# Optimization experiments

Measured on AMD Instinct MI355X. Metric: run time of the kernel, lower is better.

Reference implementation:

```python
import jax, jax.numpy as jnp
import numpy as np

N_NODES = 50000
N_EDGES = 600000
D_IN = 128
D_OUT = 128
P_DROP = 0.1
BN_EPS = 1e-5


def setup_inputs() -> dict:
    key = jax.random.key(0)
    ks = jax.random.split(key, 6)
    x = jax.random.normal(ks[0], (N_NODES, D_IN), dtype=jnp.float32)
    weight = jax.random.normal(ks[1], (D_IN, D_OUT), dtype=jnp.float32) * (1.0 / np.sqrt(D_IN))
    bias = jnp.zeros((D_OUT,), dtype=jnp.float32)
    gamma = jnp.ones((D_OUT,), dtype=jnp.float32)
    beta = jnp.zeros((D_OUT,), dtype=jnp.float32)
    dropout_u = jax.random.uniform(ks[2], (N_NODES, D_OUT), dtype=jnp.float32)
    edge_index = jax.random.randint(ks[3], (2, N_EDGES), 0, N_NODES, dtype=jnp.int64)
    return {"x": x, "weight": weight, "bias": bias, "gamma": gamma,
            "beta": beta, "dropout_u": dropout_u, "edge_index": edge_index}


def reference(x, weight, bias, gamma, beta, dropout_u, edge_index):
    N = x.shape[0]
    # --- GCNConv (add_self_loops=True, symmetric normalization) ---
    loop = jnp.arange(N, dtype=edge_index.dtype)
    src = jnp.concatenate([edge_index[0], loop])  # [E+N]
    dst = jnp.concatenate([edge_index[1], loop])  # [E+N]
    xw = x @ weight                               # [N, D_OUT] small GEMM
    deg = jnp.zeros((N,), dtype=xw.dtype).at[dst].add(1.0)
    dinv = jnp.where(deg > 0, jax.lax.rsqrt(jnp.maximum(deg, 1.0)), 0.0)
    norm = dinv[src] * dinv[dst]                  # [E+N]
    msgs = xw[src] * norm[:, None]                # gather: [E+N, D_OUT]
    z = jax.ops.segment_sum(msgs, dst, num_segments=N) + bias
    # --- activation -> BatchNorm (training stats) -> dropout ---
    z = jax.nn.relu(z)
    mean = jnp.mean(z, axis=0)
    var = jnp.mean((z - mean) ** 2, axis=0)       # biased var, as BN uses
    z = (z - mean) * jax.lax.rsqrt(var + BN_EPS) * gamma + beta
    keep = (dropout_u > P_DROP).astype(z.dtype)
    z = z * keep * (1.0 / (1.0 - P_DROP))
    return z.astype(x.dtype)
```

## Files before the change

kernel.cpp:

```cpp
#include <hip/hip_runtime.h>
#include <cstdint>
#include <cstddef>

#define D 128
#define P_DROP 0.1f
#define INV_KEEP (1.0f / 0.9f)
#define BN_EPS 1e-5f

typedef __attribute__((ext_vector_type(8))) short bf16x8;
typedef __attribute__((ext_vector_type(4))) float f32x4;

__device__ __forceinline__ unsigned f2bf(float f) {
    unsigned u = __float_as_uint(f);
    return (u + 0x7fffu + ((u >> 16) & 1u)) >> 16;
}
__device__ __forceinline__ float bf_lo(unsigned v) { return __uint_as_float(v << 16); }
__device__ __forceinline__ float bf_hi(unsigned v) { return __uint_as_float(v & 0xffff0000u); }

__global__ void k_init(int* __restrict__ hist, int N,
                       float* __restrict__ bnacc,
                       unsigned short* __restrict__ xwb) {
    int stride = gridDim.x * blockDim.x;
    int i0 = blockIdx.x * blockDim.x + threadIdx.x;
    for (int i = i0; i < N; i += stride) hist[i] = 0;
    for (int i = i0; i < 2048; i += stride) bnacc[i] = 0.f;
    if (i0 < 64) ((unsigned*)(xwb + (size_t)N * D))[i0] = 0u;
}

__global__ void k_hist(const int* __restrict__ dst, int* __restrict__ hist, int E) {
    int i = blockIdx.x * blockDim.x + threadIdx.x;
    if (i < E) atomicAdd(&hist[dst[i]], 1);
}

__global__ void k_scanA(const int* __restrict__ hist, int* __restrict__ tmp,
                        int* __restrict__ blocksum, int N) {
    __shared__ int sd[256];
    int tid = threadIdx.x;
    int i = blockIdx.x * 256 + tid;
    sd[tid] = (i < N) ? ((hist[i] + 7) & ~7) : 0;
    __syncthreads();
    for (int o = 1; o < 256; o <<= 1) {
        int t = (tid >= o) ? sd[tid - o] : 0;
        __syncthreads();
        sd[tid] += t;
        __syncthreads();
    }
    tmp[i] = sd[tid];
    if (tid == 255) blocksum[blockIdx.x] = sd[255];
}

__global__ void k_scanBC(const int* __restrict__ tmp, const int* __restrict__ blocksum,
                         const int* __restrict__ hist,
                         int* __restrict__ rowptr, int* __restrict__ cursor,
                         unsigned short* __restrict__ ssrc,
                         int N, int NBLK, int sent) {
    __shared__ int sd[256];
    int tid = threadIdx.x;
    int b = blockIdx.x;
    sd[tid] = (tid < NBLK && tid < b) ? blocksum[tid] : 0;
    __syncthreads();
    for (int o = 128; o > 0; o >>= 1) {
        if (tid < o) sd[tid] += sd[tid + o];
        __syncthreads();
    }
    int boff = sd[0];
    int i = b * 256 + tid;
    if (i < N) {
        int deg = hist[i];
        int pd = (deg + 7) & ~7;
        int r = tmp[i] + boff - pd;
        rowptr[i] = r;
        cursor[i] = r;
        for (int k = deg; k < pd; ++k) ssrc[r + k] = (unsigned short)sent;
    }
}

__global__ void k_place(const int* __restrict__ src, const int* __restrict__ dst,
                        int* __restrict__ cursor, unsigned short* __restrict__ ssrc, int E) {
    int i = blockIdx.x * blockDim.x + threadIdx.x;
    if (i < E) {
        int d = dst[i];
        int p = atomicAdd(&cursor[d], 1);
        ssrc[p] = (unsigned short)src[i];
    }
}

__global__ __launch_bounds__(256) void k_gemm(
    const float* __restrict__ x, const float* __restrict__ w,
    const int* __restrict__ hist, unsigned short* __restrict__ xwb,
    float* __restrict__ dinv, int N) {
    __shared__ unsigned short xs[64][136];
    __shared__ unsigned short wt[128][136];
    int tid = threadIdx.x;
    int row0 = blockIdx.x * 64;

#pragma unroll
    for (int i = 0; i < 32; ++i) {
        int flat = tid + i * 256;
        int n = flat & 127;
        int kp = flat >> 7;
        float a0 = w[(size_t)(2 * kp) * D + n];
        float a1 = w[(size_t)(2 * kp + 1) * D + n];
        *(unsigned*)&wt[n][2 * kp] = f2bf(a0) | (f2bf(a1) << 16);
    }
#pragma unroll
    for (int i = 0; i < 8; ++i) {
        int flat = tid + i * 256;
        int r = flat >> 5;
        int kq = flat & 31;
        int row = row0 + r;
        float4 v = (row < N) ? *(const float4*)&x[(size_t)row * D + kq * 4]
                             : make_float4(0.f, 0.f, 0.f, 0.f);
        uint2 pk;
        pk.x = f2bf(v.x) | (f2bf(v.y) << 16);
        pk.y = f2bf(v.z) | (f2bf(v.w) << 16);
        *(uint2*)&xs[r][kq * 4] = pk;
    }
    __syncthreads();

    int wv = tid >> 6, lane = tid & 63;
    int l15 = lane & 15, quad = lane >> 4;
    int mrow = wv * 16 + l15;
    f32x4 acc[8];
#pragma unroll
    for (int t = 0; t < 8; ++t) acc[t] = (f32x4){0.f, 0.f, 0.f, 0.f};
#pragma unroll
    for (int k0 = 0; k0 < D; k0 += 32) {
        bf16x8 af = *(bf16x8*)&xs[mrow][k0 + quad * 8];
#pragma unroll
        for (int nt = 0; nt < 8; ++nt) {
            bf16x8 bfr = *(bf16x8*)&wt[nt * 16 + l15][k0 + quad * 8];
            acc[nt] = __builtin_amdgcn_mfma_f32_16x16x32_bf16(af, bfr, acc[nt], 0, 0, 0);
        }
    }
#pragma unroll
    for (int reg = 0; reg < 4; ++reg) {
        int node = row0 + wv * 16 + quad * 4 + reg;
        if (node < N) {
            float dv = rsqrtf((float)(hist[node] + 1));
            if (l15 == 0) dinv[node] = dv;
#pragma unroll
            for (int nt = 0; nt < 8; ++nt) {
                float val = acc[nt][reg] * dv;
                xwb[(size_t)node * D + nt * 16 + l15] = (unsigned short)f2bf(val);
            }
        }
    }
}

__global__ __launch_bounds__(256) void k_aggregate(
    const unsigned short* __restrict__ xwb, const float* __restrict__ dinv,
    const unsigned short* __restrict__ ssrc, const int* __restrict__ rowptr,
    const int* __restrict__ hist, const float* __restrict__ bias,
    float* __restrict__ y, float* __restrict__ bnacc, int N) {
    int tid = threadIdx.x;
    int lane = tid & 63;
    int wv = tid >> 6;
    int w0 = blockIdx.x * 4 + wv;
    int totw = gridDim.x * 4;
    float2 b2 = *(const float2*)(bias + lane * 2);
    float s0 = 0.f, s1 = 0.f, q0 = 0.f, q1 = 0.f;

    int n = w0;
    int baseC = 0, degC = 0, vsC = 0;
    if (n < N) {
        baseC = rowptr[n];
        degC = hist[n];
        vsC = (int)ssrc[baseC + lane];
    }
    int np = n + totw;
    int baseP = 0, degP = 0;
    if (np < N) { baseP = rowptr[np]; degP = hist[np]; }

    while (n < N) {
        int nn = __builtin_amdgcn_readfirstlane(n);
        int vsP = 0;
        if (np < N) vsP = (int)ssrc[baseP + lane];
        int n2 = np + totw;
        int base2 = 0, deg2 = 0;
        if (n2 < N) { base2 = rowptr[n2]; deg2 = hist[n2]; }
        unsigned sv = *(const unsigned*)(xwb + (size_t)nn * D + lane * 2);
        int pdeg = (degC + 7) & ~7;
        float a0 = 0.f, a1 = 0.f;
        int lim0 = min(64, pdeg);
        for (int j0 = 0; j0 < lim0; j0 += 8) {
            unsigned vr[8];
#pragma unroll
            for (int j = 0; j < 8; ++j) {
                int idx = __builtin_amdgcn_readlane(vsC, j0 + j);
                vr[j] = *(const unsigned*)(xwb + (size_t)idx * D + lane * 2);
            }
#pragma unroll
            for (int j = 0; j < 8; ++j) { a0 += bf_lo(vr[j]); a1 += bf_hi(vr[j]); }
        }
        for (int c0 = 64; c0 < pdeg; c0 += 64) {
            int vs2 = (int)ssrc[baseC + c0 + lane];
            int lim = min(64, pdeg - c0);
            for (int j0 = 0; j0 < lim; j0 += 8) {
                unsigned vr[8];
#pragma unroll
                for (int j = 0; j < 8; ++j) {
                    int idx = __builtin_amdgcn_readlane(vs2, j0 + j);
                    vr[j] = *(const unsigned*)(xwb + (size_t)idx * D + lane * 2);
                }
#pragma unroll
                for (int j = 0; j < 8; ++j) { a0 += bf_lo(vr[j]); a1 += bf_hi(vr[j]); }
            }
        }
        a0 += bf_lo(sv); a1 += bf_hi(sv);
        float dv = dinv[nn];
        float z0 = fmaxf(fmaf(a0, dv, b2.x), 0.f);
        float z1 = fmaxf(fmaf(a1, dv, b2.y), 0.f);
        *(float2*)(y + (size_t)nn * D + lane * 2) = make_float2(z0, z1);
        s0 += z0; s1 += z1; q0 += z0 * z0; q1 += z1 * z1;
        n = np; baseC = baseP; degC = degP; vsC = vsP;
        np = n2; baseP = base2; degP = deg2;
    }

    __shared__ float red[256][4];
    red[tid][0] = s0; red[tid][1] = s1; red[tid][2] = q0; red[tid][3] = q1;
    __syncthreads();
    int o = tid;
    int col = o & 127;
    int l = col >> 1;
    int si = ((o >= 128) ? 2 : 0) + (col & 1);
    float acc = red[0 * 64 + l][si] + red[1 * 64 + l][si] +
                red[2 * 64 + l][si] + red[3 * 64 + l][si];
    atomicAdd(bnacc + 256 * (blockIdx.x & 7) + o, acc);
}

__global__ __launch_bounds__(256) void k_finalize(
    float* __restrict__ out, const float* __restrict__ u,
    const float* __restrict__ bnacc, const float* __restrict__ gamma,
    const float* __restrict__ beta, int total4, float invN) {
    __shared__ float sc[128], sh[128];
    int tid = threadIdx.x;
    if (tid < 128) {
        float sm = 0.f, sq = 0.f;
#pragma unroll
        for (int k = 0; k < 8; ++k) {
            sm += bnacc[k * 256 + tid];
            sq += bnacc[k * 256 + 128 + tid];
        }
        float mean = sm * invN;
        float var = fmaxf(sq * invN - mean * mean, 0.f);
        float s = gamma[tid] * rsqrtf(var + BN_EPS);
        sc[tid] = s;
        sh[tid] = beta[tid] - mean * s;
    }
    __syncthreads();
    int stride = gridDim.x * 256;
    for (int i = blockIdx.x * 256 + tid; i < total4; i += stride) {
        float4 v = ((const float4*)out)[i];
        float4 uu = ((const float4*)u)[i];
        int c = (i & 31) * 4;
        v.x = fmaf(v.x, sc[c],     sh[c])     * (uu.x > P_DROP ? INV_KEEP : 0.f);
        v.y = fmaf(v.y, sc[c + 1], sh[c + 1]) * (uu.y > P_DROP ? INV_KEEP : 0.f);
        v.z = fmaf(v.z, sc[c + 2], sh[c + 2]) * (uu.z > P_DROP ? INV_KEEP : 0.f);
        v.w = fmaf(v.w, sc[c + 3], sh[c + 3]) * (uu.w > P_DROP ? INV_KEEP : 0.f);
        ((float4*)out)[i] = v;
    }
}

extern "C" void kernel_launch(void* const* d_in, const int* in_sizes, int n_in,
                              void* d_out, int out_size, void* d_ws, size_t ws_size,
                              hipStream_t stream) {
    const float* x      = (const float*)d_in[0];
    const float* weight = (const float*)d_in[1];
    const float* bias   = (const float*)d_in[2];
    const float* gamma  = (const float*)d_in[3];
    const float* beta   = (const float*)d_in[4];
    const float* du     = (const float*)d_in[5];
    const int*   eidx   = (const int*)d_in[6];
    float* out = (float*)d_out;

    const int N = in_sizes[0] / D;
    const int E = in_sizes[6] / 2;
    const int* esrc = eidx;
    const int* edst = eidx + E;

    char* p = (char*)d_ws;
    auto alloc = [&](size_t bytes) {
        char* q = p;
        p += (bytes + 255) & ~(size_t)255;
        return q;
    };
    unsigned short* xwb = (unsigned short*)alloc((size_t)(N + 1) * D * sizeof(unsigned short));
    int*   hist     = (int*)alloc((size_t)N * sizeof(int));
    int*   cursor   = (int*)alloc((size_t)N * sizeof(int));
    int*   rowptr   = (int*)alloc((size_t)N * sizeof(int));
    const int NBLK = (N + 255) / 256;
    int*   tmp      = (int*)alloc((size_t)NBLK * 256 * sizeof(int));
    int*   blocksum = (int*)alloc((size_t)NBLK * sizeof(int));
    const int PS = E + 7 * N + 128;
    unsigned short* ssrc = (unsigned short*)alloc((size_t)PS * sizeof(unsigned short));
    float* dinv     = (float*)alloc((size_t)N * sizeof(float));
    float* bnacc    = (float*)alloc(8 * 256 * sizeof(float));

    const int EB = (E + 255) / 256;
    const int total4 = N * (D / 4);

    hipLaunchKernelGGL(k_init, dim3(256), dim3(256), 0, stream,
                       hist, N, bnacc, xwb);
    hipLaunchKernelGGL(k_hist, dim3(EB), dim3(256), 0, stream, edst, hist, E);
    hipLaunchKernelGGL(k_scanA, dim3(NBLK), dim3(256), 0, stream, hist, tmp, blocksum, N);
    hipLaunchKernelGGL(k_scanBC, dim3(NBLK), dim3(256), 0, stream,
                       tmp, blocksum, hist, rowptr, cursor, ssrc, N, NBLK, N);
    hipLaunchKernelGGL(k_place, dim3(EB), dim3(256), 0, stream, esrc, edst, cursor, ssrc, E);
    hipLaunchKernelGGL(k_gemm, dim3((N + 63) / 64), dim3(256), 0, stream,
                       x, weight, hist, xwb, dinv, N);
    hipLaunchKernelGGL(k_aggregate, dim3(1024), dim3(256), 0, stream,
                       xwb, dinv, ssrc, rowptr, hist, bias, out, bnacc, N);
    hipLaunchKernelGGL(k_finalize, dim3(2048), dim3(256), 0, stream,
                       out, du, bnacc, gamma, beta, total4, 1.0f / (float)N);
}
```

Before: 217.2 us.

## Pre-convert weight to bf16 once and partition edge placement by destination range

The fp32 weight is converted and transposed to bf16 a single time in the init kernel. Each GEMM block then loads it with 16-byte vector copies instead of re-reading and converting strided fp32 values in all ~780 blocks. Edge placement now runs as 8 groups of blocks, each scanning every edge but only placing those whose destination falls in its eighth of the node range. The aim is to keep the cursor atomics and ssrc scatter writes for each group within a smaller, more cache-local region, at the cost of reading the edge list 8 times.

```diff
diff --git a/kernel.cpp b/kernel.cpp
--- a/kernel.cpp
+++ b/kernel.cpp
@@ -19,11 +19,17 @@
 
 __global__ void k_init(int* __restrict__ hist, int N,
                        float* __restrict__ bnacc,
-                       unsigned short* __restrict__ xwb) {
+                       unsigned short* __restrict__ xwb,
+                       const float* __restrict__ w,
+                       unsigned short* __restrict__ wbf) {
     int stride = gridDim.x * blockDim.x;
     int i0 = blockIdx.x * blockDim.x + threadIdx.x;
     for (int i = i0; i < N; i += stride) hist[i] = 0;
     for (int i = i0; i < 2048; i += stride) bnacc[i] = 0.f;
+    for (int i = i0; i < 16384; i += stride) {
+        int n = i & 127, k = i >> 7;
+        wbf[n * 128 + k] = (unsigned short)f2bf(w[(size_t)k * 128 + n]);
+    }
     if (i0 < 64) ((unsigned*)(xwb + (size_t)N * D))[i0] = 0u;
 }
 
@@ -76,17 +82,24 @@
 }
 
 __global__ void k_place(const int* __restrict__ src, const int* __restrict__ dst,
-                        int* __restrict__ cursor, unsigned short* __restrict__ ssrc, int E) {
-    int i = blockIdx.x * blockDim.x + threadIdx.x;
-    if (i < E) {
+                        int* __restrict__ cursor, unsigned short* __restrict__ ssrc,
+                        int E, int N) {
+    int g = blockIdx.x & 7;
+    int gid = blockIdx.x >> 3;
+    int G = gridDim.x >> 3;
+    int lo = (int)((long long)N * g >> 3);
+    int hi = (int)((long long)N * (g + 1) >> 3);
+    for (int i = gid * blockDim.x + threadIdx.x; i < E; i += G * blockDim.x) {
         int d = dst[i];
-        int p = atomicAdd(&cursor[d], 1);
-        ssrc[p] = (unsigned short)src[i];
+        if (d >= lo && d < hi) {
+            int p = atomicAdd(&cursor[d], 1);
+            ssrc[p] = (unsigned short)src[i];
+        }
     }
 }
 
 __global__ __launch_bounds__(256) void k_gemm(
-    const float* __restrict__ x, const float* __restrict__ w,
+    const float* __restrict__ x, const unsigned short* __restrict__ wbf,
     const int* __restrict__ hist, unsigned short* __restrict__ xwb,
     float* __restrict__ dinv, int N) {
     __shared__ unsigned short xs[64][136];
@@ -95,13 +108,11 @@
     int row0 = blockIdx.x * 64;
 
 #pragma unroll
-    for (int i = 0; i < 32; ++i) {
+    for (int i = 0; i < 8; ++i) {
         int flat = tid + i * 256;
-        int n = flat & 127;
-        int kp = flat >> 7;
-        float a0 = w[(size_t)(2 * kp) * D + n];
-        float a1 = w[(size_t)(2 * kp + 1) * D + n];
-        *(unsigned*)&wt[n][2 * kp] = f2bf(a0) | (f2bf(a1) << 16);
+        int n = flat >> 4;
+        int ko = (flat & 15) * 8;
+        *(uint4*)&wt[n][ko] = *(const uint4*)&wbf[n * 128 + ko];
     }
 #pragma unroll
     for (int i = 0; i < 8; ++i) {
@@ -296,19 +307,20 @@
     unsigned short* ssrc = (unsigned short*)alloc((size_t)PS * sizeof(unsigned short));
     float* dinv     = (float*)alloc((size_t)N * sizeof(float));
     float* bnacc    = (float*)alloc(8 * 256 * sizeof(float));
+    unsigned short* wbf = (unsigned short*)alloc(16384 * sizeof(unsigned short));
 
     const int EB = (E + 255) / 256;
     const int total4 = N * (D / 4);
 
     hipLaunchKernelGGL(k_init, dim3(256), dim3(256), 0, stream,
-                       hist, N, bnacc, xwb);
+                       hist, N, bnacc, xwb, weight, wbf);
     hipLaunchKernelGGL(k_hist, dim3(EB), dim3(256), 0, stream, edst, hist, E);
     hipLaunchKernelGGL(k_scanA, dim3(NBLK), dim3(256), 0, stream, hist, tmp, blocksum, N);
     hipLaunchKernelGGL(k_scanBC, dim3(NBLK), dim3(256), 0, stream,
                        tmp, blocksum, hist, rowptr, cursor, ssrc, N, NBLK, N);
-    hipLaunchKernelGGL(k_place, dim3(EB), dim3(256), 0, stream, esrc, edst, cursor, ssrc, E);
+    hipLaunchKernelGGL(k_place, dim3(1024), dim3(256), 0, stream, esrc, edst, cursor, ssrc, E, N);
     hipLaunchKernelGGL(k_gemm, dim3((N + 63) / 64), dim3(256), 0, stream,
-                       x, weight, hist, xwb, dinv, N);
+                       x, wbf, hist, xwb, dinv, N);
     hipLaunchKernelGGL(k_aggregate, dim3(1024), dim3(256), 0, stream,
                        xwb, dinv, ssrc, rowptr, hist, bias, out, bnacc, N);
     hipLaunchKernelGGL(k_finalize, dim3(2048), dim3(256), 0, stream,
```

Result: faster. 211.1 us (-2.8%).
